# Performance work log

Hardware: AMD Instinct MI355X
Metric: run time of the kernel (lower is better)

The kernel has to match this reference:

```python
import jax, jax.numpy as jnp
import numpy as np

WINDOW_SIZE = 11
SIGMA = 1.5
C1 = 0.01 ** 2
C2 = 0.03 ** 2


def _make_window(channel, dtype=jnp.float32):
    # Faithful to torch `gaussian`: center at window_size/2 (= 5.5 for ws=11)
    x = np.arange(WINDOW_SIZE, dtype=np.float64)
    g = np.exp(-((x - WINDOW_SIZE / 2) ** 2) / (2.0 * SIGMA ** 2))
    g = (g / g.sum()).astype(np.float32)
    w2d = np.outer(g, g)  # (ws, ws)
    w = np.broadcast_to(w2d, (channel, 1, WINDOW_SIZE, WINDOW_SIZE)).copy()
    return jnp.asarray(w, dtype=dtype)


def _dwconv(x, w, channel):
    pad = WINDOW_SIZE // 2
    return jax.lax.conv_general_dilated(
        x, w,
        window_strides=(1, 1),
        padding=[(pad, pad), (pad, pad)],
        dimension_numbers=("NCHW", "OIHW", "NCHW"),
        feature_group_count=channel,
    )


def setup_inputs() -> dict:
    key = jax.random.key(0)
    k1, k2 = jax.random.split(key)
    B, C, H, W = 16, 3, 512, 512
    img1 = jax.random.uniform(k1, (B, C, H, W), dtype=jnp.float32)
    img2 = jax.random.uniform(k2, (B, C, H, W), dtype=jnp.float32)
    return {"img1": img1, "img2": img2}


def reference(img1, img2):
    channel = img1.shape[1]
    window = _make_window(channel, img1.dtype)

    mu1 = _dwconv(img1, window, channel)
    mu2 = _dwconv(img2, window, channel)
    mu1_sq = mu1 * mu1
    mu2_sq = mu2 * mu2
    mu1_mu2 = mu1 * mu2

    sigma1_sq = _dwconv(img1 * img1, window, channel) - mu1_sq
    sigma2_sq = _dwconv(img2 * img2, window, channel) - mu2_sq
    sigma12 = _dwconv(img1 * img2, window, channel) - mu1_mu2

    numerator = (2 * mu1_mu2 + C1) * (2 * sigma12 + C2)
    denominator = (mu1_sq + mu2_sq + C1) * (sigma1_sq + sigma2_sq + C2)
    ssim_map = numerator / denominator
    return jnp.mean(ssim_map)  # size_average=True
```

## Files before the change

kernel.cpp:

```cpp
#include <hip/hip_runtime.h>
#include <cmath>


#define IMG_H 512
#define IMG_W 512
#define STRIPE 32
#define NSTR (IMG_H / STRIPE)
#define NPLANES 48
#define NBLOCKS (NPLANES * NSTR)
#define SSIM_C1 (0.01f * 0.01f)
#define SSIM_C2 (0.03f * 0.03f)

typedef float f32x2 __attribute__((ext_vector_type(2)));

struct W2x11 { float2 w[11]; };

__launch_bounds__(512, 2)
__global__ void ssim_main(const float* __restrict__ img1,
                          const float* __restrict__ img2,
                          float* __restrict__ blockSums, W2x11 wv) {
    __shared__ float2 tb[2][528];
    __shared__ float red[8];

    const int x = threadIdx.x;
    const int bid = blockIdx.x;
    const int plane = bid >> 4;
    const int stripe = bid & (NSTR - 1);
    const int y0 = stripe * STRIPE;
    const size_t base = (size_t)plane * (IMG_H * IMG_W);

    if (x < 10) {
        const int col = (x < 5) ? x : (x + 512);
        tb[0][col] = make_float2(0.f, 0.f);
        tb[1][col] = make_float2(0.f, 0.f);
    }

    f32x2 rAB[11], rSP[11];
    float acc = 0.f;

    float pa = 0.f, pb = 0.f;
    {
        const int r0 = y0 - 5;
        if (r0 >= 0) {
            pa = img1[base + (size_t)r0 * IMG_W + x];
            pb = img2[base + (size_t)r0 * IMG_W + x];
        }
    }

    int buf = 0;
#pragma unroll 1
    for (int c = 0; c < 4; ++c) {
#pragma unroll
        for (int j = 0; j < 11; ++j) {
            const int i = c * 11 + j;
            if (i < 42) {
                tb[buf][x + 5] = make_float2(pa, pb);
                pa = 0.f; pb = 0.f;
                const int rn = y0 - 4 + i;
                if (i + 1 < 42 && rn >= 0 && rn < IMG_H) {
                    pa = img1[base + (size_t)rn * IMG_W + x];
                    pb = img2[base + (size_t)rn * IMG_W + x];
                }
                __syncthreads();
                f32x2 hAB = {0.f, 0.f}, hSP = {0.f, 0.f};
#pragma unroll
                for (int k = 0; k < 11; ++k) {
                    const float2 t = tb[buf][x + k];
                    f32x2 ab; ab.x = t.x; ab.y = t.y;
                    f32x2 sp;
                    sp.x = fmaf(t.y, t.y, t.x * t.x);
                    sp.y = t.x * t.y;
                    f32x2 w2; w2.x = wv.w[k].x; w2.y = wv.w[k].y;
                    hAB = __builtin_elementwise_fma(w2, ab, hAB);
                    hSP = __builtin_elementwise_fma(w2, sp, hSP);
                }
                rAB[j] = hAB; rSP[j] = hSP;

                if (i >= 10) {
                    f32x2 vAB = {0.f, 0.f}, vSP = {0.f, 0.f};
#pragma unroll
                    for (int k = 0; k < 11; ++k) {
                        const int s = (j + 1 + k) % 11;
                        f32x2 w2; w2.x = wv.w[k].x; w2.y = wv.w[k].y;
                        vAB = __builtin_elementwise_fma(w2, rAB[s], vAB);
                        vSP = __builtin_elementwise_fma(w2, rSP[s], vSP);
                    }
                    const float vA = vAB.x, vB = vAB.y;
                    const float vS = vSP.x, vP = vSP.y;
                    const float mu11 = vA * vA;
                    const float mu22 = vB * vB;
                    const float mu12 = vA * vB;
                    const float num = fmaf(2.f, mu12, SSIM_C1) *
                                      fmaf(2.f, vP - mu12, SSIM_C2);
                    const float d1  = mu11 + mu22;
                    const float den = (d1 + SSIM_C1) * ((vS - d1) + SSIM_C2);
                    acc = fmaf(num, __builtin_amdgcn_rcpf(den), acc);
                }
                buf ^= 1;
            }
        }
    }

#pragma unroll
    for (int off = 32; off >= 1; off >>= 1)
        acc += __shfl_down(acc, off, 64);
    const int wave = x >> 6, lane = x & 63;
    if (lane == 0) red[wave] = acc;
    __syncthreads();
    if (x == 0) {
        float s = 0.f;
#pragma unroll
        for (int k = 0; k < 8; ++k) s += red[k];
        blockSums[bid] = s;
    }
}

__global__ void ssim_reduce(const float* __restrict__ bs,
                            float* __restrict__ out) {
    __shared__ double red[4];
    const int t = threadIdx.x;
    double a = 0.0;
    for (int idx = t; idx < NBLOCKS; idx += 256) a += (double)bs[idx];
#pragma unroll
    for (int off = 32; off >= 1; off >>= 1)
        a += __shfl_down(a, off, 64);
    const int wave = t >> 6, lane = t & 63;
    if (lane == 0) red[wave] = a;
    __syncthreads();
    if (t == 0) {
        const double s = red[0] + red[1] + red[2] + red[3];
        out[0] = (float)(s / (double)((double)NPLANES * IMG_H * IMG_W));
    }
}

extern "C" void kernel_launch(void* const* d_in, const int* in_sizes, int n_in,
                              void* d_out, int out_size, void* d_ws, size_t ws_size,
                              hipStream_t stream) {
    const float* img1 = (const float*)d_in[0];
    const float* img2 = (const float*)d_in[1];
    float* out = (float*)d_out;
    float* bs = (float*)d_ws;

    W2x11 wv;
    double g[11], s = 0.0;
    for (int i = 0; i < 11; ++i) {
        const double d = (double)i - 5.5;
        g[i] = exp(-(d * d) / (2.0 * 1.5 * 1.5));
        s += g[i];
    }
    for (int i = 0; i < 11; ++i) {
        const float w = (float)(g[i] / s);
        wv.w[i] = make_float2(w, w);
    }

    ssim_main<<<NBLOCKS, 512, 0, stream>>>(img1, img2, bs, wv);
    ssim_reduce<<<1, 256, 0, stream>>>(bs, out);
}
```

Before: 149.5 us.

## Tile each plane into 128x128 blocks with 128-thread workgroups and halos

Changes decomposition from full-width 32-row stripes with 512 threads to 128x128 tiles processed by 128-thread blocks, each streaming 138 rows with a 10-column halo loaded by extra threads. Vertical halo overhead drops from about 42/32 rows to 138/128, but horizontal halo loads and redundant horizontal convolution work grow, and each block has far fewer threads, so latency hiding depends on more resident blocks. The grid stays at 768 blocks, and per-row syncs become cheaper with fewer waves per block.

```diff
diff --git a/kernel.cpp b/kernel.cpp
--- a/kernel.cpp
+++ b/kernel.cpp
@@ -4,10 +4,14 @@
 
 #define IMG_H 512
 #define IMG_W 512
-#define STRIPE 32
-#define NSTR (IMG_H / STRIPE)
+#define BR 128
+#define BC 128
+#define SR (BR + 10)
+#define SC (BC + 10)
+#define NRB (IMG_H / BR)
+#define NCB (IMG_W / BC)
 #define NPLANES 48
-#define NBLOCKS (NPLANES * NSTR)
+#define NBLOCKS (NPLANES * NRB * NCB)
 #define SSIM_C1 (0.01f * 0.01f)
 #define SSIM_C2 (0.03f * 0.03f)
 
@@ -15,61 +19,66 @@
 
 struct W2x11 { float2 w[11]; };
 
-__launch_bounds__(512, 2)
+__launch_bounds__(128, 6)
 __global__ void ssim_main(const float* __restrict__ img1,
                           const float* __restrict__ img2,
                           float* __restrict__ blockSums, W2x11 wv) {
-    __shared__ float2 tb[2][528];
-    __shared__ float red[8];
+    __shared__ float2 tb[2][SC + 2];
+    __shared__ float red[2];
 
-    const int x = threadIdx.x;
+    const int t = threadIdx.x;
     const int bid = blockIdx.x;
     const int plane = bid >> 4;
-    const int stripe = bid & (NSTR - 1);
-    const int y0 = stripe * STRIPE;
+    const int rb = (bid >> 2) & 3;
+    const int cb = bid & 3;
+    const int y0 = rb * BR;
+    const int x0 = cb * BC;
     const size_t base = (size_t)plane * (IMG_H * IMG_W);
 
-    if (x < 10) {
-        const int col = (x < 5) ? x : (x + 512);
-        tb[0][col] = make_float2(0.f, 0.f);
-        tb[1][col] = make_float2(0.f, 0.f);
-    }
+    const int c1 = x0 - 5 + t;
+    const int c2 = x0 + BC - 5 + t;
+    const bool c1ok = (c1 >= 0) && (c1 < IMG_W);
+    const bool e2 = (t < 10);
+    const bool c2ok = e2 && (c2 < IMG_W);
 
     f32x2 rAB[11], rSP[11];
     float acc = 0.f;
 
-    float pa = 0.f, pb = 0.f;
+    float pa = 0.f, pb = 0.f, qa = 0.f, qb = 0.f;
     {
         const int r0 = y0 - 5;
         if (r0 >= 0) {
-            pa = img1[base + (size_t)r0 * IMG_W + x];
-            pb = img2[base + (size_t)r0 * IMG_W + x];
+            const size_t rowb = base + (size_t)r0 * IMG_W;
+            if (c1ok) { pa = img1[rowb + c1]; pb = img2[rowb + c1]; }
+            if (c2ok) { qa = img1[rowb + c2]; qb = img2[rowb + c2]; }
         }
     }
 
     int buf = 0;
 #pragma unroll 1
-    for (int c = 0; c < 4; ++c) {
+    for (int c = 0; c < 13; ++c) {
 #pragma unroll
         for (int j = 0; j < 11; ++j) {
             const int i = c * 11 + j;
-            if (i < 42) {
-                tb[buf][x + 5] = make_float2(pa, pb);
-                pa = 0.f; pb = 0.f;
+            if (i < SR) {
+                tb[buf][t] = make_float2(pa, pb);
+                if (e2) tb[buf][BC + t] = make_float2(qa, qb);
+                pa = 0.f; pb = 0.f; qa = 0.f; qb = 0.f;
                 const int rn = y0 - 4 + i;
-                if (i + 1 < 42 && rn >= 0 && rn < IMG_H) {
-                    pa = img1[base + (size_t)rn * IMG_W + x];
-                    pb = img2[base + (size_t)rn * IMG_W + x];
+                if (i + 1 < SR && rn >= 0 && rn < IMG_H) {
+                    const size_t rowb = base + (size_t)rn * IMG_W;
+                    if (c1ok) { pa = img1[rowb + c1]; pb = img2[rowb + c1]; }
+                    if (c2ok) { qa = img1[rowb + c2]; qb = img2[rowb + c2]; }
                 }
                 __syncthreads();
                 f32x2 hAB = {0.f, 0.f}, hSP = {0.f, 0.f};
 #pragma unroll
                 for (int k = 0; k < 11; ++k) {
-                    const float2 t = tb[buf][x + k];
-                    f32x2 ab; ab.x = t.x; ab.y = t.y;
+                    const float2 v = tb[buf][t + k];
+                    f32x2 ab; ab.x = v.x; ab.y = v.y;
                     f32x2 sp;
-                    sp.x = fmaf(t.y, t.y, t.x * t.x);
-                    sp.y = t.x * t.y;
+                    sp.x = fmaf(v.y, v.y, v.x * v.x);
+                    sp.y = v.x * v.y;
                     f32x2 w2; w2.x = wv.w[k].x; w2.y = wv.w[k].y;
                     hAB = __builtin_elementwise_fma(w2, ab, hAB);
                     hSP = __builtin_elementwise_fma(w2, sp, hSP);
@@ -104,15 +113,10 @@
 #pragma unroll
     for (int off = 32; off >= 1; off >>= 1)
         acc += __shfl_down(acc, off, 64);
-    const int wave = x >> 6, lane = x & 63;
+    const int wave = t >> 6, lane = t & 63;
     if (lane == 0) red[wave] = acc;
     __syncthreads();
-    if (x == 0) {
-        float s = 0.f;
-#pragma unroll
-        for (int k = 0; k < 8; ++k) s += red[k];
-        blockSums[bid] = s;
-    }
+    if (t == 0) blockSums[bid] = red[0] + red[1];
 }
 
 __global__ void ssim_reduce(const float* __restrict__ bs,
@@ -153,6 +157,6 @@
         wv.w[i] = make_float2(w, w);
     }
 
-    ssim_main<<<NBLOCKS, 512, 0, stream>>>(img1, img2, bs, wv);
+    ssim_main<<<NBLOCKS, 128, 0, stream>>>(img1, img2, bs, wv);
     ssim_reduce<<<1, 256, 0, stream>>>(bs, out);
 }
```

After: 180.9 us. 21.0% more time.

## Swap to vertical-first separable conv with two-row batching and float4 LDS horizontal pass

Applied to the files above, without the earlier changes.

Reorders the separable Gaussian so each thread first does the vertical 11-tap pass on raw per-column values held in a register ring, then writes the vertical results to LDS. Two rows are handled per barrier: threads 0-255 and 256-511 each take one row and compute two adjacent output columns from shared float4 loads. This halves the number of __syncthreads and removes the redundant per-tap square/product computation in the horizontal pass. In exchange it uses four LDS planes instead of one double-buffered tile, making the LDS footprint larger, and the indexing is more complex.

```diff
diff --git a/kernel.cpp b/kernel.cpp
--- a/kernel.cpp
+++ b/kernel.cpp
@@ -19,7 +19,8 @@
 __global__ void ssim_main(const float* __restrict__ img1,
                           const float* __restrict__ img2,
                           float* __restrict__ blockSums, W2x11 wv) {
-    __shared__ float2 tb[2][528];
+    __shared__ __align__(16) float2 abL[2][2][532];
+    __shared__ __align__(16) float2 spL[2][2][532];
     __shared__ float red[8];
 
     const int x = threadIdx.x;
@@ -31,72 +32,159 @@
 
     if (x < 10) {
         const int col = (x < 5) ? x : (x + 512);
-        tb[0][col] = make_float2(0.f, 0.f);
-        tb[1][col] = make_float2(0.f, 0.f);
+#pragma unroll
+        for (int d = 0; d < 2; ++d)
+#pragma unroll
+            for (int r = 0; r < 2; ++r) {
+                abL[d][r][col] = make_float2(0.f, 0.f);
+                spL[d][r][col] = make_float2(0.f, 0.f);
+            }
     }
 
     f32x2 rAB[11], rSP[11];
     float acc = 0.f;
 
-    float pa = 0.f, pb = 0.f;
+    float pa0 = 0.f, pb0 = 0.f, pa1 = 0.f, pb1 = 0.f;
     {
-        const int r0 = y0 - 5;
+        const int r0 = y0 - 5, r1 = y0 - 4;
         if (r0 >= 0) {
-            pa = img1[base + (size_t)r0 * IMG_W + x];
-            pb = img2[base + (size_t)r0 * IMG_W + x];
+            pa0 = img1[base + (size_t)r0 * IMG_W + x];
+            pb0 = img2[base + (size_t)r0 * IMG_W + x];
+        }
+        if (r1 >= 0) {
+            pa1 = img1[base + (size_t)r1 * IMG_W + x];
+            pb1 = img2[base + (size_t)r1 * IMG_W + x];
         }
     }
 
     int buf = 0;
 #pragma unroll 1
-    for (int c = 0; c < 4; ++c) {
-#pragma unroll
-        for (int j = 0; j < 11; ++j) {
-            const int i = c * 11 + j;
-            if (i < 42) {
-                tb[buf][x + 5] = make_float2(pa, pb);
-                pa = 0.f; pb = 0.f;
-                const int rn = y0 - 4 + i;
-                if (i + 1 < 42 && rn >= 0 && rn < IMG_H) {
-                    pa = img1[base + (size_t)rn * IMG_W + x];
-                    pb = img2[base + (size_t)rn * IMG_W + x];
-                }
-                __syncthreads();
-                f32x2 hAB = {0.f, 0.f}, hSP = {0.f, 0.f};
-#pragma unroll
-                for (int k = 0; k < 11; ++k) {
-                    const float2 t = tb[buf][x + k];
-                    f32x2 ab; ab.x = t.x; ab.y = t.y;
+    for (int c = 0; c < 2; ++c) {
+#pragma unroll
+        for (int jp = 0; jp < 11; ++jp) {
+            const int p = c * 11 + jp;
+            if (p < 21) {
+                const int j1 = (2 * jp) % 11;
+                const int j2 = (2 * jp + 1) % 11;
+                {
+                    f32x2 ab; ab.x = pa0; ab.y = pb0;
                     f32x2 sp;
-                    sp.x = fmaf(t.y, t.y, t.x * t.x);
-                    sp.y = t.x * t.y;
-                    f32x2 w2; w2.x = wv.w[k].x; w2.y = wv.w[k].y;
-                    hAB = __builtin_elementwise_fma(w2, ab, hAB);
-                    hSP = __builtin_elementwise_fma(w2, sp, hSP);
-                }
-                rAB[j] = hAB; rSP[j] = hSP;
-
-                if (i >= 10) {
+                    sp.x = fmaf(pb0, pb0, pa0 * pa0);
+                    sp.y = pa0 * pb0;
+                    rAB[j1] = ab; rSP[j1] = sp;
+                }
+                if (p >= 5) {
                     f32x2 vAB = {0.f, 0.f}, vSP = {0.f, 0.f};
 #pragma unroll
                     for (int k = 0; k < 11; ++k) {
-                        const int s = (j + 1 + k) % 11;
+                        const int s = (2 * jp + 1 + k) % 11;
                         f32x2 w2; w2.x = wv.w[k].x; w2.y = wv.w[k].y;
                         vAB = __builtin_elementwise_fma(w2, rAB[s], vAB);
                         vSP = __builtin_elementwise_fma(w2, rSP[s], vSP);
                     }
-                    const float vA = vAB.x, vB = vAB.y;
-                    const float vS = vSP.x, vP = vSP.y;
-                    const float mu11 = vA * vA;
-                    const float mu22 = vB * vB;
-                    const float mu12 = vA * vB;
-                    const float num = fmaf(2.f, mu12, SSIM_C1) *
-                                      fmaf(2.f, vP - mu12, SSIM_C2);
-                    const float d1  = mu11 + mu22;
-                    const float den = (d1 + SSIM_C1) * ((vS - d1) + SSIM_C2);
-                    acc = fmaf(num, __builtin_amdgcn_rcpf(den), acc);
-                }
-                buf ^= 1;
+                    abL[buf][0][x + 5] = make_float2(vAB.x, vAB.y);
+                    spL[buf][0][x + 5] = make_float2(vSP.x, vSP.y);
+                }
+                {
+                    f32x2 ab; ab.x = pa1; ab.y = pb1;
+                    f32x2 sp;
+                    sp.x = fmaf(pb1, pb1, pa1 * pa1);
+                    sp.y = pa1 * pb1;
+                    rAB[j2] = ab; rSP[j2] = sp;
+                }
+                if (p >= 5) {
+                    f32x2 vAB = {0.f, 0.f}, vSP = {0.f, 0.f};
+#pragma unroll
+                    for (int k = 0; k < 11; ++k) {
+                        const int s = (2 * jp + 2 + k) % 11;
+                        f32x2 w2; w2.x = wv.w[k].x; w2.y = wv.w[k].y;
+                        vAB = __builtin_elementwise_fma(w2, rAB[s], vAB);
+                        vSP = __builtin_elementwise_fma(w2, rSP[s], vSP);
+                    }
+                    abL[buf][1][x + 5] = make_float2(vAB.x, vAB.y);
+                    spL[buf][1][x + 5] = make_float2(vSP.x, vSP.y);
+                }
+                pa0 = 0.f; pb0 = 0.f; pa1 = 0.f; pb1 = 0.f;
+                if (p + 1 < 21) {
+                    const int rn0 = y0 - 5 + 2 * p + 2;
+                    const int rn1 = rn0 + 1;
+                    if (rn0 >= 0 && rn0 < IMG_H) {
+                        pa0 = img1[base + (size_t)rn0 * IMG_W + x];
+                        pb0 = img2[base + (size_t)rn0 * IMG_W + x];
+                    }
+                    if (rn1 >= 0 && rn1 < IMG_H) {
+                        pa1 = img1[base + (size_t)rn1 * IMG_W + x];
+                        pb1 = img2[base + (size_t)rn1 * IMG_W + x];
+                    }
+                }
+                if (p >= 5) {
+                    __syncthreads();
+                    const int sel = x >> 8;
+                    const int u = x & 255;
+                    const float2* Ap = abL[buf][sel];
+                    const float2* Sp = spL[buf][sel];
+                    f32x2 hAB0 = {0.f, 0.f}, hAB1 = {0.f, 0.f};
+                    f32x2 hSP0 = {0.f, 0.f}, hSP1 = {0.f, 0.f};
+#pragma unroll
+                    for (int m = 0; m < 6; ++m) {
+                        const float4 q = *(const float4*)(&Ap[2 * u + 2 * m]);
+                        f32x2 lo; lo.x = q.x; lo.y = q.y;
+                        f32x2 hi; hi.x = q.z; hi.y = q.w;
+                        f32x2 w2;
+                        w2.x = wv.w[2 * m].x; w2.y = wv.w[2 * m].y;
+                        hAB0 = __builtin_elementwise_fma(w2, lo, hAB0);
+                        hAB1 = __builtin_elementwise_fma(w2, hi, hAB1);
+                        if (2 * m + 1 <= 10) {
+                            w2.x = wv.w[2 * m + 1].x; w2.y = wv.w[2 * m + 1].y;
+                            hAB0 = __builtin_elementwise_fma(w2, hi, hAB0);
+                        }
+                        if (2 * m - 1 >= 0) {
+                            w2.x = wv.w[2 * m - 1].x; w2.y = wv.w[2 * m - 1].y;
+                            hAB1 = __builtin_elementwise_fma(w2, lo, hAB1);
+                        }
+                    }
+#pragma unroll
+                    for (int m = 0; m < 6; ++m) {
+                        const float4 q = *(const float4*)(&Sp[2 * u + 2 * m]);
+                        f32x2 lo; lo.x = q.x; lo.y = q.y;
+                        f32x2 hi; hi.x = q.z; hi.y = q.w;
+                        f32x2 w2;
+                        w2.x = wv.w[2 * m].x; w2.y = wv.w[2 * m].y;
+                        hSP0 = __builtin_elementwise_fma(w2, lo, hSP0);
+                        hSP1 = __builtin_elementwise_fma(w2, hi, hSP1);
+                        if (2 * m + 1 <= 10) {
+                            w2.x = wv.w[2 * m + 1].x; w2.y = wv.w[2 * m + 1].y;
+                            hSP0 = __builtin_elementwise_fma(w2, hi, hSP0);
+                        }
+                        if (2 * m - 1 >= 0) {
+                            w2.x = wv.w[2 * m - 1].x; w2.y = wv.w[2 * m - 1].y;
+                            hSP1 = __builtin_elementwise_fma(w2, lo, hSP1);
+                        }
+                    }
+                    {
+                        const float vA = hAB0.x, vB = hAB0.y;
+                        const float vS = hSP0.x, vP = hSP0.y;
+                        const float mu11 = vA * vA, mu22 = vB * vB;
+                        const float mu12 = vA * vB;
+                        const float num = fmaf(2.f, mu12, SSIM_C1) *
+                                          fmaf(2.f, vP - mu12, SSIM_C2);
+                        const float d1  = mu11 + mu22;
+                        const float den = (d1 + SSIM_C1) * ((vS - d1) + SSIM_C2);
+                        acc = fmaf(num, __builtin_amdgcn_rcpf(den), acc);
+                    }
+                    {
+                        const float vA = hAB1.x, vB = hAB1.y;
+                        const float vS = hSP1.x, vP = hSP1.y;
+                        const float mu11 = vA * vA, mu22 = vB * vB;
+                        const float mu12 = vA * vB;
+                        const float num = fmaf(2.f, mu12, SSIM_C1) *
+                                          fmaf(2.f, vP - mu12, SSIM_C2);
+                        const float d1  = mu11 + mu22;
+                        const float den = (d1 + SSIM_C1) * ((vS - d1) + SSIM_C2);
+                        acc = fmaf(num, __builtin_amdgcn_rcpf(den), acc);
+                    }
+                    buf ^= 1;
+                }
             }
         }
     }
```

After: 159.9 us. +6.9%, slower.

## Use per-wave LDS row buffers with redundant halos to drop block barriers

Applied to the files above, without the earlier changes.

Each 64-lane wave now keeps its own LDS row buffer that holds its 64 columns plus a 5-column halo on each side. The halo is loaded from global memory by ten extra lanes per wave, so waves no longer share a row buffer. This lets the per-row __syncthreads and the double buffer go away, since a wave only reads data it wrote itself. The cost is some redundant, divergent halo loads, plus a reliance on in-order LDS access within a wavefront with no explicit barrier or fence.

```diff
diff --git a/kernel.cpp b/kernel.cpp
--- a/kernel.cpp
+++ b/kernel.cpp
@@ -18,59 +18,64 @@
 __launch_bounds__(512, 2)
 __global__ void ssim_main(const float* __restrict__ img1,
                           const float* __restrict__ img2,
-                          float* __restrict__ blockSums, W2x11 wv) {
-    __shared__ float2 tb[2][528];
+                          float* __restrict__ blockSums, W2x11 wvp) {
+    __shared__ float2 wbuf[8][76];
     __shared__ float red[8];
 
     const int x = threadIdx.x;
+    const int wid = x >> 6;
+    const int lane = x & 63;
     const int bid = blockIdx.x;
     const int plane = bid >> 4;
     const int stripe = bid & (NSTR - 1);
     const int y0 = stripe * STRIPE;
     const size_t base = (size_t)plane * (IMG_H * IMG_W);
 
-    if (x < 10) {
-        const int col = (x < 5) ? x : (x + 512);
-        tb[0][col] = make_float2(0.f, 0.f);
-        tb[1][col] = make_float2(0.f, 0.f);
-    }
+    const bool hlane = (lane < 10);
+    const int hc = (wid << 6) + ((lane < 5) ? (lane - 5) : (lane + 59));
+    const bool hok = hlane && (hc >= 0) && (hc < IMG_W);
+    const int hslot = (lane < 5) ? lane : (lane + 64);
+    const int hcc = hok ? hc : 0;
 
     f32x2 rAB[11], rSP[11];
     float acc = 0.f;
 
-    float pa = 0.f, pb = 0.f;
+    float pa = 0.f, pb = 0.f, qa = 0.f, qb = 0.f;
     {
         const int r0 = y0 - 5;
         if (r0 >= 0) {
-            pa = img1[base + (size_t)r0 * IMG_W + x];
-            pb = img2[base + (size_t)r0 * IMG_W + x];
+            const size_t rb = base + (size_t)r0 * IMG_W;
+            pa = img1[rb + x];
+            pb = img2[rb + x];
+            if (hok) { qa = img1[rb + hcc]; qb = img2[rb + hcc]; }
         }
     }
 
-    int buf = 0;
 #pragma unroll 1
     for (int c = 0; c < 4; ++c) {
 #pragma unroll
         for (int j = 0; j < 11; ++j) {
             const int i = c * 11 + j;
             if (i < 42) {
-                tb[buf][x + 5] = make_float2(pa, pb);
-                pa = 0.f; pb = 0.f;
+                wbuf[wid][lane + 5] = make_float2(pa, pb);
+                if (hlane) wbuf[wid][hslot] = make_float2(qa, qb);
+                pa = 0.f; pb = 0.f; qa = 0.f; qb = 0.f;
                 const int rn = y0 - 4 + i;
                 if (i + 1 < 42 && rn >= 0 && rn < IMG_H) {
-                    pa = img1[base + (size_t)rn * IMG_W + x];
-                    pb = img2[base + (size_t)rn * IMG_W + x];
+                    const size_t rb = base + (size_t)rn * IMG_W;
+                    pa = img1[rb + x];
+                    pb = img2[rb + x];
+                    if (hok) { qa = img1[rb + hcc]; qb = img2[rb + hcc]; }
                 }
-                __syncthreads();
                 f32x2 hAB = {0.f, 0.f}, hSP = {0.f, 0.f};
 #pragma unroll
                 for (int k = 0; k < 11; ++k) {
-                    const float2 t = tb[buf][x + k];
+                    const float2 t = wbuf[wid][lane + k];
                     f32x2 ab; ab.x = t.x; ab.y = t.y;
                     f32x2 sp;
                     sp.x = fmaf(t.y, t.y, t.x * t.x);
                     sp.y = t.x * t.y;
-                    f32x2 w2; w2.x = wv.w[k].x; w2.y = wv.w[k].y;
+                    f32x2 w2; w2.x = wvp.w[k].x; w2.y = wvp.w[k].y;
                     hAB = __builtin_elementwise_fma(w2, ab, hAB);
                     hSP = __builtin_elementwise_fma(w2, sp, hSP);
                 }
@@ -81,7 +86,7 @@
 #pragma unroll
                     for (int k = 0; k < 11; ++k) {
                         const int s = (j + 1 + k) % 11;
-                        f32x2 w2; w2.x = wv.w[k].x; w2.y = wv.w[k].y;
+                        f32x2 w2; w2.x = wvp.w[k].x; w2.y = wvp.w[k].y;
                         vAB = __builtin_elementwise_fma(w2, rAB[s], vAB);
                         vSP = __builtin_elementwise_fma(w2, rSP[s], vSP);
                     }
@@ -96,7 +101,6 @@
                     const float den = (d1 + SSIM_C1) * ((vS - d1) + SSIM_C2);
                     acc = fmaf(num, __builtin_amdgcn_rcpf(den), acc);
                 }
-                buf ^= 1;
             }
         }
     }
@@ -104,8 +108,7 @@
 #pragma unroll
     for (int off = 32; off >= 1; off >>= 1)
         acc += __shfl_down(acc, off, 64);
-    const int wave = x >> 6, lane = x & 63;
-    if (lane == 0) red[wave] = acc;
+    if (lane == 0) red[wid] = acc;
     __syncthreads();
     if (x == 0) {
         float s = 0.f;
```

Result: slower. 156.1 us (+4.4%).
